# Kernel optimization log

Measured on AMD Instinct MI355X. Metric: run time of the kernel, lower is better.

The kernel has to match this reference:

```python
import jax, jax.numpy as jnp
import numpy as np

N_E = 8192
E_DIM = 256
BETA = 0.25


def setup_inputs() -> dict:
    key = jax.random.key(0)
    k1, k2 = jax.random.split(key)
    z = jax.random.normal(k1, (16, 1024, E_DIM), dtype=jnp.float32)
    emb = jax.random.uniform(k2, (N_E, E_DIM), dtype=jnp.float32,
                             minval=-1.0 / N_E, maxval=1.0 / N_E)
    return {"z": z, "emb": emb}


def reference(z, emb):
    zf = z.reshape(-1, E_DIM)                       # [N, D]
    # squared L2 distances: ||z||^2 + ||e||^2 - 2 z.e  -> [N, n_e]
    d = (jnp.sum(zf * zf, axis=1, keepdims=True)
         + jnp.sum(emb * emb, axis=1)
         - 2.0 * jnp.einsum('nd,kd->nk', zf, emb))
    idx = jnp.argmin(d, axis=1).reshape(z.shape[:-1])  # [B, T]
    z_q = emb[idx]                                   # [B, T, D]
    loss = (BETA * jnp.mean((jax.lax.stop_gradient(z_q) - z) ** 2)
            + jnp.mean((z_q - jax.lax.stop_gradient(z)) ** 2))
    z_q = z + jax.lax.stop_gradient(z_q - z)         # straight-through
    return z_q, loss, idx
```

## Files before the change

kernel.cpp:

```cpp
#include <hip/hip_runtime.h>
#include <hip/hip_bf16.h>

#define D 256
#define BM 32
#define CAPG 92
#define MARGIN 2.5e-4f

typedef short bf16x8 __attribute__((ext_vector_type(8)));
typedef float f32x4 __attribute__((ext_vector_type(4)));

__device__ inline unsigned short f2bf(float f) {
    __hip_bfloat16 h = __float2bfloat16(f);
    return *reinterpret_cast<unsigned short*>(&h);
}
__device__ inline unsigned f2ord(float f) {
    unsigned u = __float_as_uint(f);
    return (u & 0x80000000u) ? ~u : (u | 0x80000000u);
}
__device__ inline float ord2f(unsigned u) {
    unsigned b = (u & 0x80000000u) ? (u ^ 0x80000000u) : ~u;
    return __uint_as_float(b);
}

__global__ __launch_bounds__(512) void vq_ebfrag(const float* __restrict__ emb,
                                                 unsigned short* __restrict__ ebf) {
    const int cb = blockIdx.x;
    const int tid = threadIdx.x;
    const int kc = tid >> 6;
    const int l = tid & 63;
    const int q = l >> 4, lm = l & 15;
    const float4* emb4 = (const float4*)emb;
    #pragma unroll
    for (int fc = 0; fc < 4; ++fc) {
        const int code = cb * 64 + fc * 16 + lm;
        float4 a = emb4[(size_t)code * 64 + kc * 8 + q * 2];
        float4 b = emb4[(size_t)code * 64 + kc * 8 + q * 2 + 1];
        ushort4 o0, o1;
        o0.x = f2bf(a.x); o0.y = f2bf(a.y); o0.z = f2bf(a.z); o0.w = f2bf(a.w);
        o1.x = f2bf(b.x); o1.y = f2bf(b.y); o1.z = f2bf(b.z); o1.w = f2bf(b.w);
        unsigned short* dst = ebf + (((size_t)(cb * 8 + kc) * 4 + fc) << 9) + l * 8;
        *(ushort4*)dst = o0;
        *(ushort4*)(dst + 4) = o1;
    }
}

__global__ __launch_bounds__(256) void vq_rownorm(const float* __restrict__ x,
                                                  float* __restrict__ out, int rows,
                                                  float* loss_zero, int* cntG) {
#pragma clang fp contract(off)
    int r = blockIdx.x * blockDim.x + threadIdx.x;
    if (r == 0 && loss_zero) loss_zero[0] = 0.f;
    if (r >= rows) return;
    if (cntG) cntG[r] = 0;
    const float4* p4 = (const float4*)(x + (size_t)r * D);
    float s = 0.f;
    for (int i = 0; i < 64; ++i) {
        float4 v = p4[i];
        s = s + v.x * v.x;
        s = s + v.y * v.y;
        s = s + v.z * v.z;
        s = s + v.w * v.w;
    }
    out[r] = s;
}

__global__ __launch_bounds__(512, 4) void vq_filter(
    const float* __restrict__ z, const unsigned short* __restrict__ ebf,
    const float* __restrict__ enorm,
    int* __restrict__ cntG, int* __restrict__ candC, float* __restrict__ candS) {
#pragma clang fp contract(off)
    __shared__ unsigned short zsh[BM][264];
    __shared__ unsigned rowmin[BM];

    const int tid = threadIdx.x;
    const int w = tid >> 6;
    const int l = tid & 63;
    const int q = l >> 4;
    const int lm = l & 15;
    const int b = blockIdx.x;
    const int rowBase = (b & 511) * BM;
    const int qt = b >> 9;

    if (tid < BM) rowmin[tid] = 0xffffffffu;

    #pragma unroll
    for (int rc = 0; rc < 4; ++rc) {
        int i4 = tid + rc * 512;
        int row = i4 >> 6, c4 = i4 & 63;
        float4 v = ((const float4*)(z + ((size_t)(rowBase + row) << 8)))[c4];
        ushort4 o;
        o.x = f2bf(v.x); o.y = f2bf(v.y); o.z = f2bf(v.z); o.w = f2bf(v.w);
        *(ushort4*)&zsh[row][c4 * 4] = o;
    }
    __syncthreads();

    for (int t = 0; t < 4; ++t) {
        const int cb = qt * 32 + t * 8 + w;
        const int codeBase = cb * 64;
        const unsigned short* fb = ebf + ((size_t)cb << 14);
        float ne[4];
        #pragma unroll
        for (int fc = 0; fc < 4; ++fc) ne[fc] = enorm[codeBase + fc * 16 + lm];

        f32x4 acc[2][4];
        #pragma unroll
        for (int a = 0; a < 2; ++a)
            #pragma unroll
            for (int c = 0; c < 4; ++c) acc[a][c] = (f32x4)0.f;

        #pragma unroll
        for (int kc = 0; kc < 8; ++kc) {
            bf16x8 af[2], bfr[4];
            af[0] = *(const bf16x8*)&zsh[lm][kc * 32 + q * 8];
            af[1] = *(const bf16x8*)&zsh[16 + lm][kc * 32 + q * 8];
            #pragma unroll
            for (int fc = 0; fc < 4; ++fc)
                bfr[fc] = *(const bf16x8*)(fb + kc * 2048 + fc * 512 + l * 8);
            #pragma unroll
            for (int fr = 0; fr < 2; ++fr)
                #pragma unroll
                for (int fc = 0; fc < 4; ++fc)
                    acc[fr][fc] = __builtin_amdgcn_mfma_f32_16x16x32_bf16(af[fr], bfr[fc], acc[fr][fc], 0, 0, 0);
        }

        f32x4 m4[2];
        #pragma unroll
        for (int fr = 0; fr < 2; ++fr) {
            #pragma unroll
            for (int e = 0; e < 4; ++e) {
                float m = 3.4e38f;
                #pragma unroll
                for (int fc = 0; fc < 4; ++fc) {
                    float s = ne[fc] - 2.0f * acc[fr][fc][e];
                    m = fminf(m, s);
                }
                m4[fr][e] = m;
                #pragma unroll
                for (int off = 1; off < 16; off <<= 1)
                    m = fminf(m, __shfl_xor(m, off));
                if (lm == 0)
                    atomicMin(&rowmin[fr * 16 + q * 4 + e], f2ord(m));
            }
        }
        #pragma unroll
        for (int fr = 0; fr < 2; ++fr) {
            uint4 u = *(const uint4*)&rowmin[fr * 16 + q * 4];
            f32x4 thr = {ord2f(u.x) + MARGIN, ord2f(u.y) + MARGIN,
                         ord2f(u.z) + MARGIN, ord2f(u.w) + MARGIN};
            #pragma unroll
            for (int e = 0; e < 4; ++e) {
                if (m4[fr][e] >= thr[e]) continue;
                int row = rowBase + fr * 16 + q * 4 + e;
                #pragma unroll
                for (int fc = 0; fc < 4; ++fc) {
                    float s = ne[fc] - 2.0f * acc[fr][fc][e];
                    if (s < thr[e]) {
                        int slot = atomicAdd(&cntG[row], 1);
                        if (slot < CAPG) {
                            candC[(size_t)row * CAPG + slot] = codeBase + fc * 16 + lm;
                            candS[(size_t)row * CAPG + slot] = s;
                        }
                    }
                }
            }
        }
    }
}

__global__ __launch_bounds__(256) void vq_rescore(
    const float* __restrict__ z, const float* __restrict__ emb,
    const float* __restrict__ znorm, const float* __restrict__ enorm,
    const int* __restrict__ cntG, const int* __restrict__ candC,
    const float* __restrict__ candS, float* __restrict__ idxf, int K) {
#pragma clang fp contract(off)
    __shared__ unsigned sapx[64];
    __shared__ unsigned sbits[64];
    __shared__ int sidx[64];
    __shared__ int ovList[64];
    __shared__ int ovCnt;

    const int tid = threadIdx.x;
    const int rowBase = blockIdx.x * 64;
    if (tid < 64) { sapx[tid] = 0xffffffffu; sbits[tid] = 0xffffffffu; sidx[tid] = 0x7fffffff; }
    if (tid == 0) ovCnt = 0;
    __syncthreads();

    const int r = tid & 63;
    const int c0 = tid >> 6;
    const int grow = rowBase + r;
    const int n = min(cntG[grow], CAPG);

    {
        float amin = 3.4e38f;
        for (int c = c0; c < n; c += 4)
            amin = fminf(amin, candS[(size_t)grow * CAPG + c]);
        atomicMin(&sapx[r], f2ord(amin));
    }
    if (tid < 64 && cntG[rowBase + tid] > CAPG) {
        int o = atomicAdd(&ovCnt, 1);
        ovList[o] = tid;
    }
    __syncthreads();

    const float Anz = znorm[grow];
    const float4* zp4 = (const float4*)(z + ((size_t)grow << 8));
    const float athr = ord2f(sapx[r]) + MARGIN;

    float bestS = 3.4e38f; int bestK = 0x7fffffff;
    for (int c = c0; c < n; c += 4) {
        if (candS[(size_t)grow * CAPG + c] > athr) continue;
        int k = candC[(size_t)grow * CAPG + c];
        const float4* ep4 = (const float4*)(emb + ((size_t)k << 8));
        float s = 0.f;
        #pragma unroll 8
        for (int d4 = 0; d4 < 64; ++d4) {
            float4 a = zp4[d4], b = ep4[d4];
            s = s + a.x * b.x;
            s = s + a.y * b.y;
            s = s + a.z * b.z;
            s = s + a.w * b.w;
        }
        float sc = (Anz + enorm[k]) - 2.0f * s;
        if (sc < bestS || (sc == bestS && k < bestK)) { bestS = sc; bestK = k; }
    }
    if (bestK != 0x7fffffff) atomicMin(&sbits[r], __float_as_uint(bestS));
    __syncthreads();

    const int nov = ovCnt;
    for (int o = 0; o < nov; ++o) {
        const int rr = ovList[o];
        const float Az = znorm[rowBase + rr];
        const float4* zr4 = (const float4*)(z + ((size_t)(rowBase + rr) << 8));
        float bS = 3.4e38f; int bK = 0x7fffffff;
        for (int k = tid; k < K; k += 256) {
            const float4* ep4 = (const float4*)(emb + ((size_t)k << 8));
            float s = 0.f;
            #pragma unroll 8
            for (int d4 = 0; d4 < 64; ++d4) {
                float4 a = zr4[d4], b = ep4[d4];
                s = s + a.x * b.x; s = s + a.y * b.y;
                s = s + a.z * b.z; s = s + a.w * b.w;
            }
            float sc = (Az + enorm[k]) - 2.0f * s;
            if (sc < bS || (sc == bS && k < bK)) { bS = sc; bK = k; }
        }
        atomicMin(&sbits[rr], __float_as_uint(bS));
        __syncthreads();
        if (__float_as_uint(bS) == sbits[rr]) atomicMin(&sidx[rr], bK);
        __syncthreads();
    }

    if (bestK != 0x7fffffff && __float_as_uint(bestS) == sbits[r])
        atomicMin(&sidx[r], bestK);
    __syncthreads();
    if (tid < 64) idxf[rowBase + tid] = (float)sidx[tid];
}

__global__ __launch_bounds__(256) void vq_gather(
    const float* __restrict__ z, const float* __restrict__ emb,
    const float* __restrict__ idxf, float* __restrict__ zq,
    float* __restrict__ loss, float scale) {
    const int tid = threadIdx.x;
    const int lane = tid & 63, w = tid >> 6;
    const int rowBase = blockIdx.x * 64;
    float lsum = 0.f;
    for (int t = 0; t < 16; ++t) {
        int gr = rowBase + w * 16 + t;
        int k = (int)idxf[gr];
        k = (k < 0) ? 0 : ((k > 8191) ? 8191 : k);
        float4 e  = ((const float4*)emb)[(size_t)k * 64 + lane];
        float4 zv = ((const float4*)z)[(size_t)gr * 64 + lane];
        ((float4*)zq)[(size_t)gr * 64 + lane] = e;
        float dx = e.x - zv.x, dy = e.y - zv.y, dz = e.z - zv.z, dw = e.w - zv.w;
        lsum = fmaf(dx, dx, lsum); lsum = fmaf(dy, dy, lsum);
        lsum = fmaf(dz, dz, lsum); lsum = fmaf(dw, dw, lsum);
    }
    #pragma unroll
    for (int off = 32; off; off >>= 1) lsum += __shfl_down(lsum, off);
    __shared__ float ps[4];
    if (lane == 0) ps[w] = lsum;
    __syncthreads();
    if (tid == 0) atomicAdd(loss, (ps[0] + ps[1] + ps[2] + ps[3]) * scale);
}

extern "C" void kernel_launch(void* const* d_in, const int* in_sizes, int n_in,
                              void* d_out, int out_size, void* d_ws, size_t ws_size,
                              hipStream_t stream) {
    const float* z   = (const float*)d_in[0];
    const float* emb = (const float*)d_in[1];
    const int N = in_sizes[0] / D;
    const int K = in_sizes[1] / D;

    float* out  = (float*)d_out;
    float* zq   = out;
    const size_t Z = (size_t)N * D;
    float* loss = out + Z;
    float* idxf = loss + 1;

    char* base = (char*)zq;
    unsigned short* ebf = (unsigned short*)base;
    float* znorm   = (float*)(base + (size_t)K * D * 2);
    float* enorm   = znorm + N;
    int* cntG      = (int*)(enorm + K);
    int* candC     = cntG + N;
    float* candS   = (float*)(candC + (size_t)N * CAPG);

    vq_ebfrag <<<K / 64, 512, 0, stream>>>(emb, ebf);
    vq_rownorm<<<(N + 255) / 256, 256, 0, stream>>>(z, znorm, N, loss, cntG);
    vq_rownorm<<<(K + 255) / 256, 256, 0, stream>>>(emb, enorm, K, nullptr, nullptr);
    vq_filter <<<(N / BM) * 4, 512, 0, stream>>>(z, ebf, enorm, cntG, candC, candS);
    vq_rescore<<<N / 64, 256, 0, stream>>>(z, emb, znorm, enorm, cntG, candC, candS, idxf, K);
    vq_gather <<<N / 64, 256, 0, stream>>>(z, emb, idxf, zq, loss,
                                           1.25f / ((float)N * (float)D));
}
```

Baseline: 219.8 us.

## Merge row-norm launches, halve filter grid split, raise MFMA wave priority

```diff
diff --git a/kernel.cpp b/kernel.cpp
--- a/kernel.cpp
+++ b/kernel.cpp
@@ -44,15 +44,19 @@
     }
 }
 
-__global__ __launch_bounds__(256) void vq_rownorm(const float* __restrict__ x,
-                                                  float* __restrict__ out, int rows,
-                                                  float* loss_zero, int* cntG) {
+__global__ __launch_bounds__(256) void vq_rownorm2(const float* __restrict__ z,
+                                                   const float* __restrict__ emb,
+                                                   float* __restrict__ znorm,
+                                                   float* __restrict__ enorm,
+                                                   int N, int K,
+                                                   float* loss_zero, int* cntG) {
 #pragma clang fp contract(off)
     int r = blockIdx.x * blockDim.x + threadIdx.x;
-    if (r == 0 && loss_zero) loss_zero[0] = 0.f;
-    if (r >= rows) return;
-    if (cntG) cntG[r] = 0;
-    const float4* p4 = (const float4*)(x + (size_t)r * D);
+    if (r == 0) loss_zero[0] = 0.f;
+    if (r >= N + K) return;
+    const float* src = (r < N) ? (z + ((size_t)r << 8)) : (emb + ((size_t)(r - N) << 8));
+    if (r < N) cntG[r] = 0;
+    const float4* p4 = (const float4*)src;
     float s = 0.f;
     for (int i = 0; i < 64; ++i) {
         float4 v = p4[i];
@@ -61,14 +65,13 @@
         s = s + v.z * v.z;
         s = s + v.w * v.w;
     }
-    out[r] = s;
+    if (r < N) znorm[r] = s; else enorm[r - N] = s;
 }
 
 __global__ __launch_bounds__(512, 4) void vq_filter(
     const float* __restrict__ z, const unsigned short* __restrict__ ebf,
     const float* __restrict__ enorm,
     int* __restrict__ cntG, int* __restrict__ candC, float* __restrict__ candS) {
-#pragma clang fp contract(off)
     __shared__ unsigned short zsh[BM][264];
     __shared__ unsigned rowmin[BM];
 
@@ -79,7 +82,7 @@
     const int lm = l & 15;
     const int b = blockIdx.x;
     const int rowBase = (b & 511) * BM;
-    const int qt = b >> 9;
+    const int half = b >> 9;
 
     if (tid < BM) rowmin[tid] = 0xffffffffu;
 
@@ -94,8 +97,8 @@
     }
     __syncthreads();
 
-    for (int t = 0; t < 4; ++t) {
-        const int cb = qt * 32 + t * 8 + w;
+    for (int t = 0; t < 8; ++t) {
+        const int cb = half * 64 + t * 8 + w;
         const int codeBase = cb * 64;
         const unsigned short* fb = ebf + ((size_t)cb << 14);
         float ne[4];
@@ -116,11 +119,13 @@
             #pragma unroll
             for (int fc = 0; fc < 4; ++fc)
                 bfr[fc] = *(const bf16x8*)(fb + kc * 2048 + fc * 512 + l * 8);
+            __builtin_amdgcn_s_setprio(1);
             #pragma unroll
             for (int fr = 0; fr < 2; ++fr)
                 #pragma unroll
                 for (int fc = 0; fc < 4; ++fc)
                     acc[fr][fc] = __builtin_amdgcn_mfma_f32_16x16x32_bf16(af[fr], bfr[fc], acc[fr][fc], 0, 0, 0);
+            __builtin_amdgcn_s_setprio(0);
         }
 
         f32x4 m4[2];
@@ -305,11 +310,10 @@
     int* candC     = cntG + N;
     float* candS   = (float*)(candC + (size_t)N * CAPG);
 
-    vq_ebfrag <<<K / 64, 512, 0, stream>>>(emb, ebf);
-    vq_rownorm<<<(N + 255) / 256, 256, 0, stream>>>(z, znorm, N, loss, cntG);
-    vq_rownorm<<<(K + 255) / 256, 256, 0, stream>>>(emb, enorm, K, nullptr, nullptr);
-    vq_filter <<<(N / BM) * 4, 512, 0, stream>>>(z, ebf, enorm, cntG, candC, candS);
-    vq_rescore<<<N / 64, 256, 0, stream>>>(z, emb, znorm, enorm, cntG, candC, candS, idxf, K);
-    vq_gather <<<N / 64, 256, 0, stream>>>(z, emb, idxf, zq, loss,
-                                           1.25f / ((float)N * (float)D));
-}
+    vq_ebfrag  <<<K / 64, 512, 0, stream>>>(emb, ebf);
+    vq_rownorm2<<<(N + K + 255) / 256, 256, 0, stream>>>(z, emb, znorm, enorm, N, K, loss, cntG);
+    vq_filter  <<<(N / BM) * 2, 512, 0, stream>>>(z, ebf, enorm, cntG, candC, candS);
+    vq_rescore <<<N / 64, 256, 0, stream>>>(z, emb, znorm, enorm, cntG, candC, candS, idxf, K);
+    vq_gather  <<<N / 64, 256, 0, stream>>>(z, emb, idxf, zq, loss,
+                                            1.25f / ((float)N * (float)D));
+}
```

Result: faster. 203.5 us (-7.4%).
